# Performance work log

Hardware: AMD Instinct MI355X
Metric: run time of the kernel (lower is better)

The kernel has to match this reference:

```python
import jax, jax.numpy as jnp
import numpy as np

B, N, F, H, E = 8, 10000, 256, 128, 320000
P_DROP = 0.5

def setup_inputs() -> dict:
    key = jax.random.key(0)
    kx, ku, kr, kc, kv, kw = jax.random.split(key, 6)
    x = jax.random.normal(kx, (B, N, F), dtype=jnp.float32)
    drop_u = jax.random.uniform(ku, (B, N, F), dtype=jnp.float32)
    rows = jax.random.randint(kr, (B, E), 0, N, dtype=jnp.int64)
    cols = jax.random.randint(kc, (B, E), 0, N, dtype=jnp.int64)
    vals = jax.random.uniform(kv, (B, E), dtype=jnp.float32)
    weight = jax.random.normal(kw, (F, H), dtype=jnp.float32)
    return {"x": x, "drop_u": drop_u, "rows": rows, "cols": cols, "vals": vals, "weight": weight}

def _spmm(rows, cols, vals, dense):
    # out[r] += vals * dense[c]  -> A @ dense for one graph
    gathered = vals[:, None] * dense[cols]          # [E, H]
    return jax.ops.segment_sum(gathered, rows, num_segments=N)  # [N, H]

def reference(x, drop_u, rows, cols, vals, weight):
    # inverted dropout, p=0.5
    mask = (drop_u > P_DROP).astype(x.dtype)
    xd = x * mask * (1.0 / (1.0 - P_DROP))          # [B, N, F]
    xw = jnp.einsum('bnf,fh->bnh', xd, weight)      # [B, N, H]
    out = jax.vmap(_spmm)(rows, cols, vals, xw)     # [B, N, H]
    return out
```

## Files before the change

### kernel.cpp

```cpp
#include <hip/hip_runtime.h>
#include <hip/hip_bf16.h>

#define DEVINL __device__ __forceinline__

constexpr int Bb = 8;
constexpr int Nn = 10000;
constexpr int Ff = 256;
constexpr int Hh = 128;
constexpr int Ee = 320000;
constexpr int Mm = Bb * Nn;

constexpr int CHUNK = 64;
constexpr int NCH = (Nn + CHUNK - 1) / CHUNK;
constexpr int CAP = 2560;
constexpr int GPB = 80;
constexpr int EPG = Ee / GPB;
constexpr int TW_BLOCKS = (Ff * Hh) / 256;

typedef __attribute__((ext_vector_type(8))) short short8;
typedef __attribute__((ext_vector_type(4))) float float4v;
typedef __attribute__((ext_vector_type(4))) unsigned short ushort4v;

DEVINL unsigned short f2b(float f) {
    unsigned int u;
    __builtin_memcpy(&u, &f, 4);
    unsigned int r = (u + 0x7fffu + ((u >> 16) & 1u)) >> 16;
    return (unsigned short)r;
}
DEVINL float i2f(int i) {
    float f;
    __builtin_memcpy(&f, &i, 4);
    return f;
}
DEVINL float lo_bf(unsigned int two) {
    unsigned int u = two << 16;
    float f;
    __builtin_memcpy(&f, &u, 4);
    return f;
}
DEVINL float hi_bf(unsigned int two) {
    unsigned int u = two & 0xffff0000u;
    float f;
    __builtin_memcpy(&f, &u, 4);
    return f;
}

__global__ __launch_bounds__(256) void bucket2_kernel(const int* __restrict__ rows,
                                                      const int* __restrict__ cols,
                                                      const float* __restrict__ vals,
                                                      int* __restrict__ cur,
                                                      int2* __restrict__ bkt,
                                                      const float* __restrict__ w,
                                                      unsigned short* __restrict__ wF) {
    int t = threadIdx.x;
    if (blockIdx.x >= Bb * GPB) {
        int idx = (blockIdx.x - Bb * GPB) * 256 + t;
        if (idx < Ff * Hh) {
            int j = idx & 7;
            int lane = (idx >> 3) & 63;
            int tt = (idx >> 9) & 7;
            int ksl = idx >> 12;
            int k = ksl * 32 + (lane >> 4) * 8 + j;
            int h = tt * 16 + (lane & 15);
            wF[idx] = f2b(w[(size_t)k * Hh + h]);
        }
        return;
    }
    __shared__ int2 sedge[EPG];
    __shared__ int lcnt[NCH];
    __shared__ int lofs[NCH];
    __shared__ int lcur[NCH];
    __shared__ int gall[NCH];
    __shared__ int wsum[4];
    int raw = blockIdx.x;
    int b = raw & 7;
    int g = raw >> 3;
    const int base = b * Ee + g * EPG;

    for (int j = t; j < NCH; j += 256) lcnt[j] = 0;
    __syncthreads();
    for (int i = t; i < EPG; i += 256)
        atomicAdd(&lcnt[rows[base + i] >> 6], 1);
    __syncthreads();
    {
        int lane = t & 63, wv = t >> 6;
        int v = (t < NCH) ? lcnt[t] : 0;
        int incl = v;
#pragma unroll
        for (int d = 1; d < 64; d <<= 1) {
            int o = __shfl_up(incl, d);
            if (lane >= d) incl += o;
        }
        if (lane == 63) wsum[wv] = incl;
        __syncthreads();
        if (t == 0) {
            int s = 0;
#pragma unroll
            for (int k = 0; k < 4; k++) { int x = wsum[k]; wsum[k] = s; s += x; }
        }
        __syncthreads();
        if (t < NCH) {
            int ex = incl - v + wsum[wv];
            lofs[t] = ex;
            lcur[t] = ex;
        }
    }
    __syncthreads();
    for (int j = t; j < NCH; j += 256) {
        int gb = atomicAdd(&cur[b * NCH + j], lcnt[j]);
        gall[j] = gb - lofs[j];
    }
    __syncthreads();
    for (int i = t; i < EPG; i += 256) {
        int r = rows[base + i];
        int c = cols[base + i];
        float vf = vals[base + i];
        int vb;
        __builtin_memcpy(&vb, &vf, 4);
        int bk = r >> 6;
        int p = atomicAdd(&lcur[bk], 1);
        sedge[p] = make_int2(((r & 63) << 26) | (c << 8) | bk, vb);
    }
    __syncthreads();
    for (int i = t; i < EPG; i += 256) {
        int2 e = sedge[i];
        int j = e.x & 0xff;
        int slot = gall[j] + i;
        if (slot < CAP)
            bkt[(size_t)(b * NCH + j) * CAP + slot] = e;
    }
}

__global__ __launch_bounds__(256, 6) void gemm_kernel(const float* __restrict__ x,
                                                      const float* __restrict__ u,
                                                      const unsigned short* __restrict__ wF,
                                                      unsigned short* __restrict__ xw) {
    __shared__ unsigned short sA[64 * 136];
    int t = threadIdx.x;
    int wave = t >> 6, lane = t & 63;
    int n = lane & 15, q = lane >> 4;
    int m0 = blockIdx.x * 64;

    float4v acc[8];
#pragma unroll
    for (int i = 0; i < 8; i++) acc[i] = {0.f, 0.f, 0.f, 0.f};

    for (int kh = 0; kh < 2; kh++) {
#pragma unroll
        for (int i = 0; i < 8; i++) {
            int idx = t + i * 256;
            int row = idx >> 5;
            int c4 = idx & 31;
            const float* xp = x + (size_t)(m0 + row) * Ff + kh * 128 + c4 * 4;
            const float* up = u + (size_t)(m0 + row) * Ff + kh * 128 + c4 * 4;
            float4 xv = *(const float4*)xp;
            float4 uv = *(const float4*)up;
            ushort4v a;
            a.x = f2b(uv.x > 0.5f ? xv.x * 2.0f : 0.0f);
            a.y = f2b(uv.y > 0.5f ? xv.y * 2.0f : 0.0f);
            a.z = f2b(uv.z > 0.5f ? xv.z * 2.0f : 0.0f);
            a.w = f2b(uv.w > 0.5f ? xv.w * 2.0f : 0.0f);
            *(ushort4v*)(&sA[row * 136 + c4 * 4]) = a;
        }
        __syncthreads();
#pragma unroll
        for (int k0 = 0; k0 < 128; k0 += 32) {
            short8 af = *(const short8*)(&sA[(wave * 16 + n) * 136 + k0 + q * 8]);
            const unsigned short* wfb = wF + (size_t)(kh * 4 + (k0 >> 5)) * 4096 + lane * 8;
#pragma unroll
            for (int tt = 0; tt < 8; tt++) {
                short8 bf = *(const short8*)(wfb + tt * 512);
                acc[tt] = __builtin_amdgcn_mfma_f32_16x16x32_bf16(af, bf, acc[tt], 0, 0, 0);
            }
        }
        __syncthreads();
    }
#pragma unroll
    for (int tt = 0; tt < 8; tt++) {
#pragma unroll
        for (int r = 0; r < 4; r++) {
            int orow = m0 + wave * 16 + q * 4 + r;
            int col = tt * 16 + n;
            xw[(size_t)orow * Hh + col] = f2b(acc[tt][r]);
        }
    }
}

__global__ __launch_bounds__(256) void spmm_kernel(const int* __restrict__ cur,
                                                   const int2* __restrict__ bkt,
                                                   const unsigned short* __restrict__ xw,
                                                   float* __restrict__ out) {
    __shared__ int2 ssort[CAP];
    __shared__ int rh[CHUNK];
    __shared__ int roff[CHUNK];
    __shared__ int rcur[CHUNK];
    int raw = blockIdx.x;
    int blk = (raw & 7) * NCH + (raw >> 3);
    int b = blk / NCH, ch = blk % NCH;
    int t = threadIdx.x, w = t >> 6, lane = t & 63;

    if (t < CHUNK) rh[t] = 0;
    __syncthreads();
    int cnt = cur[blk];
    if (cnt > CAP) cnt = CAP;
    const int2* pe = bkt + (size_t)blk * CAP;

    for (int i = t; i < cnt; i += 256)
        atomicAdd(&rh[((unsigned)pe[i].x) >> 26], 1);
    __syncthreads();
    if (w == 0) {
        int v = rh[lane];
        int s = v;
#pragma unroll
        for (int d = 1; d < 64; d <<= 1) {
            int o = __shfl_up(s, d);
            if (lane >= d) s += o;
        }
        roff[lane] = s - v;
        rcur[lane] = s - v;
    }
    __syncthreads();
    for (int i = t; i < cnt; i += 256) {
        int2 e = pe[i];
        int p = atomicAdd(&rcur[((unsigned)e.x) >> 26], 1);
        ssort[p] = make_int2(e.x & 0x3FFF00, e.y);
    }
    __syncthreads();

    const char* xwb = (const char*)(xw + (size_t)b * Nn * Hh);
    int lane4 = lane * 4;
    for (int rr = 0; rr < 16; rr++) {
        int rl = w * 16 + rr;
        int r = ch * CHUNK + rl;
        if (r >= Nn) break;
        int off = roff[rl];
        int rcnt = rh[rl];

        float a0[4], a1[4];
#pragma unroll
        for (int k = 0; k < 4; k++) { a0[k] = 0.f; a1[k] = 0.f; }

        int mn = rcnt & ~3;
        for (int i = 0; i < mn; i += 4) {
#pragma unroll
            for (int k = 0; k < 4; k++) {
                int2 e = ssort[off + i + k];
                unsigned int two = *(const unsigned int*)(xwb + (unsigned)(e.x + lane4));
                float v = i2f(e.y);
                a0[k] += v * lo_bf(two);
                a1[k] += v * hi_bf(two);
            }
        }
        for (int i = mn; i < rcnt; i++) {
            int2 e = ssort[off + i];
            unsigned int two = *(const unsigned int*)(xwb + (unsigned)(e.x + lane4));
            float v = i2f(e.y);
            a0[i - mn] += v * lo_bf(two);
            a1[i - mn] += v * hi_bf(two);
        }
        float s0 = (a0[0] + a0[1]) + (a0[2] + a0[3]);
        float s1 = (a1[0] + a1[1]) + (a1[2] + a1[3]);
        float2 res;
        res.x = s0;
        res.y = s1;
        *(float2*)(out + ((size_t)b * Nn + r) * Hh + lane * 2) = res;
    }
}

extern "C" void kernel_launch(void* const* d_in, const int* in_sizes, int n_in,
                              void* d_out, int out_size, void* d_ws, size_t ws_size,
                              hipStream_t stream) {
    const float* x    = (const float*)d_in[0];
    const float* du   = (const float*)d_in[1];
    const int*   rows = (const int*)d_in[2];
    const int*   cols = (const int*)d_in[3];
    const float* vals = (const float*)d_in[4];
    const float* w    = (const float*)d_in[5];
    float*       out  = (float*)d_out;

    char* p = (char*)d_ws;
    unsigned short* xw = (unsigned short*)p; p += (size_t)Mm * Hh * 2;
    unsigned short* wF = (unsigned short*)p; p += (size_t)Ff * Hh * 2;
    int* cur   = (int*)p; p += (size_t)Bb * NCH * 4;
    int2* bkt  = (int2*)p; p += (size_t)Bb * NCH * CAP * 8;

    hipMemsetAsync(cur, 0, (size_t)Bb * NCH * 4, stream);
    bucket2_kernel<<<Bb * GPB + TW_BLOCKS, 256, 0, stream>>>(rows, cols, vals, cur, bkt, w, wF);
    gemm_kernel<<<Mm / 64, 256, 0, stream>>>(x, du, wF, xw);
    spmm_kernel<<<Bb * NCH, 256, 0, stream>>>(cur, bkt, xw, out);
}
```

Baseline: 295.4 us.

## Fuse edge bucketing and dropout GEMM into one heterogeneous kernel launch

```diff
diff --git a/kernel.cpp b/kernel.cpp
--- a/kernel.cpp
+++ b/kernel.cpp
@@ -15,7 +15,9 @@
 constexpr int CAP = 2560;
 constexpr int GPB = 80;
 constexpr int EPG = Ee / GPB;
-constexpr int TW_BLOCKS = (Ff * Hh) / 256;
+constexpr int BUCKET_BLOCKS = Bb * GPB;
+constexpr int GEMM_BLOCKS = Mm / 64;
+constexpr int DYN_LDS = 34560;
 
 typedef __attribute__((ext_vector_type(8))) short short8;
 typedef __attribute__((ext_vector_type(4))) float float4v;
@@ -45,101 +47,103 @@
     return f;
 }
 
-__global__ __launch_bounds__(256) void bucket2_kernel(const int* __restrict__ rows,
-                                                      const int* __restrict__ cols,
-                                                      const float* __restrict__ vals,
-                                                      int* __restrict__ cur,
-                                                      int2* __restrict__ bkt,
-                                                      const float* __restrict__ w,
-                                                      unsigned short* __restrict__ wF) {
+__global__ __launch_bounds__(256) void pack_kernel(const float* __restrict__ w,
+                                                   unsigned short* __restrict__ wF) {
+    int idx = blockIdx.x * 256 + threadIdx.x;
+    if (idx < Ff * Hh) {
+        int j = idx & 7;
+        int lane = (idx >> 3) & 63;
+        int tt = (idx >> 9) & 7;
+        int ksl = idx >> 12;
+        int k = ksl * 32 + (lane >> 4) * 8 + j;
+        int h = tt * 16 + (lane & 15);
+        wF[idx] = f2b(w[(size_t)k * Hh + h]);
+    }
+}
+
+__global__ __launch_bounds__(256, 4) void fused_kernel(const int* __restrict__ rows,
+                                                       const int* __restrict__ cols,
+                                                       const float* __restrict__ vals,
+                                                       int* __restrict__ cur,
+                                                       int2* __restrict__ bkt,
+                                                       const float* __restrict__ x,
+                                                       const float* __restrict__ u,
+                                                       const unsigned short* __restrict__ wF,
+                                                       unsigned short* __restrict__ xw) {
+    extern __shared__ char dyn[];
     int t = threadIdx.x;
-    if (blockIdx.x >= Bb * GPB) {
-        int idx = (blockIdx.x - Bb * GPB) * 256 + t;
-        if (idx < Ff * Hh) {
-            int j = idx & 7;
-            int lane = (idx >> 3) & 63;
-            int tt = (idx >> 9) & 7;
-            int ksl = idx >> 12;
-            int k = ksl * 32 + (lane >> 4) * 8 + j;
-            int h = tt * 16 + (lane & 15);
-            wF[idx] = f2b(w[(size_t)k * Hh + h]);
+
+    if (blockIdx.x < BUCKET_BLOCKS) {
+        int2* sedge = (int2*)dyn;
+        int* lcnt = (int*)(dyn + EPG * 8);
+        int* lofs = lcnt + NCH;
+        int* lcur = lofs + NCH;
+        int* gall = lcur + NCH;
+        int* wsum = gall + NCH;
+        int raw = blockIdx.x;
+        int b = raw & 7;
+        int g = raw >> 3;
+        const int base = b * Ee + g * EPG;
+
+        for (int j = t; j < NCH; j += 256) lcnt[j] = 0;
+        __syncthreads();
+        for (int i = t; i < EPG; i += 256)
+            atomicAdd(&lcnt[rows[base + i] >> 6], 1);
+        __syncthreads();
+        {
+            int lane = t & 63, wv = t >> 6;
+            int v = (t < NCH) ? lcnt[t] : 0;
+            int incl = v;
+#pragma unroll
+            for (int d = 1; d < 64; d <<= 1) {
+                int o = __shfl_up(incl, d);
+                if (lane >= d) incl += o;
+            }
+            if (lane == 63) wsum[wv] = incl;
+            __syncthreads();
+            if (t == 0) {
+                int s = 0;
+#pragma unroll
+                for (int k = 0; k < 4; k++) { int xx = wsum[k]; wsum[k] = s; s += xx; }
+            }
+            __syncthreads();
+            if (t < NCH) {
+                int ex = incl - v + wsum[wv];
+                lofs[t] = ex;
+                lcur[t] = ex;
+            }
+        }
+        __syncthreads();
+        for (int j = t; j < NCH; j += 256) {
+            int gb = atomicAdd(&cur[b * NCH + j], lcnt[j]);
+            gall[j] = gb - lofs[j];
+        }
+        __syncthreads();
+        for (int i = t; i < EPG; i += 256) {
+            int r = rows[base + i];
+            int c = cols[base + i];
+            float vf = vals[base + i];
+            int vb;
+            __builtin_memcpy(&vb, &vf, 4);
+            int bk = r >> 6;
+            int p = atomicAdd(&lcur[bk], 1);
+            sedge[p] = make_int2(((r & 63) << 26) | (c << 8) | bk, vb);
+        }
+        __syncthreads();
+        for (int i = t; i < EPG; i += 256) {
+            int2 e = sedge[i];
+            int j = e.x & 0xff;
+            int slot = gall[j] + i;
+            if (slot < CAP)
+                bkt[(size_t)(b * NCH + j) * CAP + slot] = e;
         }
         return;
     }
-    __shared__ int2 sedge[EPG];
-    __shared__ int lcnt[NCH];
-    __shared__ int lofs[NCH];
-    __shared__ int lcur[NCH];
-    __shared__ int gall[NCH];
-    __shared__ int wsum[4];
-    int raw = blockIdx.x;
-    int b = raw & 7;
-    int g = raw >> 3;
-    const int base = b * Ee + g * EPG;
-
-    for (int j = t; j < NCH; j += 256) lcnt[j] = 0;
-    __syncthreads();
-    for (int i = t; i < EPG; i += 256)
-        atomicAdd(&lcnt[rows[base + i] >> 6], 1);
-    __syncthreads();
-    {
-        int lane = t & 63, wv = t >> 6;
-        int v = (t < NCH) ? lcnt[t] : 0;
-        int incl = v;
-#pragma unroll
-        for (int d = 1; d < 64; d <<= 1) {
-            int o = __shfl_up(incl, d);
-            if (lane >= d) incl += o;
-        }
-        if (lane == 63) wsum[wv] = incl;
-        __syncthreads();
-        if (t == 0) {
-            int s = 0;
-#pragma unroll
-            for (int k = 0; k < 4; k++) { int x = wsum[k]; wsum[k] = s; s += x; }
-        }
-        __syncthreads();
-        if (t < NCH) {
-            int ex = incl - v + wsum[wv];
-            lofs[t] = ex;
-            lcur[t] = ex;
-        }
-    }
-    __syncthreads();
-    for (int j = t; j < NCH; j += 256) {
-        int gb = atomicAdd(&cur[b * NCH + j], lcnt[j]);
-        gall[j] = gb - lofs[j];
-    }
-    __syncthreads();
-    for (int i = t; i < EPG; i += 256) {
-        int r = rows[base + i];
-        int c = cols[base + i];
-        float vf = vals[base + i];
-        int vb;
-        __builtin_memcpy(&vb, &vf, 4);
-        int bk = r >> 6;
-        int p = atomicAdd(&lcur[bk], 1);
-        sedge[p] = make_int2(((r & 63) << 26) | (c << 8) | bk, vb);
-    }
-    __syncthreads();
-    for (int i = t; i < EPG; i += 256) {
-        int2 e = sedge[i];
-        int j = e.x & 0xff;
-        int slot = gall[j] + i;
-        if (slot < CAP)
-            bkt[(size_t)(b * NCH + j) * CAP + slot] = e;
-    }
-}
-
-__global__ __launch_bounds__(256, 6) void gemm_kernel(const float* __restrict__ x,
-                                                      const float* __restrict__ u,
-                                                      const unsigned short* __restrict__ wF,
-                                                      unsigned short* __restrict__ xw) {
-    __shared__ unsigned short sA[64 * 136];
-    int t = threadIdx.x;
+
+    unsigned short* sA = (unsigned short*)dyn;
     int wave = t >> 6, lane = t & 63;
     int n = lane & 15, q = lane >> 4;
-    int m0 = blockIdx.x * 64;
+    int m0 = (blockIdx.x - BUCKET_BLOCKS) * 64;
 
     float4v acc[8];
 #pragma unroll
@@ -285,7 +289,8 @@
     int2* bkt  = (int2*)p; p += (size_t)Bb * NCH * CAP * 8;
 
     hipMemsetAsync(cur, 0, (size_t)Bb * NCH * 4, stream);
-    bucket2_kernel<<<Bb * GPB + TW_BLOCKS, 256, 0, stream>>>(rows, cols, vals, cur, bkt, w, wF);
-    gemm_kernel<<<Mm / 64, 256, 0, stream>>>(x, du, wF, xw);
+    pack_kernel<<<(Ff * Hh + 255) / 256, 256, 0, stream>>>(w, wF);
+    fused_kernel<<<BUCKET_BLOCKS + GEMM_BLOCKS, 256, DYN_LDS, stream>>>(
+        rows, cols, vals, cur, bkt, x, du, wF, xw);
     spmm_kernel<<<Bb * NCH, 256, 0, stream>>>(cur, bkt, xw, out);
 }
```

New measurement: 278.5 us. -5.7%, faster.
